# Performance work log

Hardware: AMD Instinct MI355X
Metric: run time of the kernel (lower is better)

Reference implementation:

```python
import jax, jax.numpy as jnp
import numpy as np

MEM_SIZE = 1_000_000
DIM = 128
BS = 256
K = 1024
TEMP = 0.07
MOM_V = 0.5
MOM_A = 0.5


def _l2norm(x, axis=-1, eps=1e-12):
    n = jnp.sqrt(jnp.sum(x * x, axis=axis, keepdims=True))
    return x / jnp.maximum(n, eps)


def setup_inputs() -> dict:
    key = jax.random.key(0)
    k1, k2, k3, k4, k5, k6 = jax.random.split(key, 6)
    video_emb = jax.random.normal(k1, (BS, DIM), dtype=jnp.float32)
    audio_emb = jax.random.normal(k2, (BS, DIM), dtype=jnp.float32)
    y = jax.random.randint(k3, (BS,), 0, MEM_SIZE, dtype=jnp.int32)
    # alias method draws over memory_size-1 items (before shifting past y)
    neg_idx = jax.random.randint(k4, (BS, K), 0, MEM_SIZE - 1, dtype=jnp.int32)
    view1_mem = _l2norm(jax.random.normal(k5, (MEM_SIZE, DIM), dtype=jnp.float32))
    view2_mem = _l2norm(jax.random.normal(k6, (MEM_SIZE, DIM), dtype=jnp.float32))
    return {
        "video_emb": video_emb,
        "audio_emb": audio_emb,
        "y": y,
        "neg_idx": neg_idx,
        "view1_mem": view1_mem,
        "view2_mem": view2_mem,
    }


def reference(video_emb, audio_emb, y, neg_idx, view1_mem, view2_mem):
    v = _l2norm(video_emb, axis=1)   # [bs, dim]
    a = _l2norm(audio_emb, axis=1)   # [bs, dim]

    # shift negative indices past the positive index y (as in sample_negatives)
    idx = neg_idx + (neg_idx >= y[:, None]).astype(neg_idx.dtype)  # [bs, K]

    # gather positives / negatives from memory banks
    v_pos = view1_mem[y]           # [bs, dim]
    a_pos = view2_mem[y]           # [bs, dim]
    v_neg = view1_mem[idx]         # [bs, K, dim]
    a_neg = view2_mem[idx]         # [bs, K, dim]

    # xModal scores (wModal=False)
    v2a_pos = jnp.einsum("bd,bd->b", a_pos, v)[:, None] / TEMP    # [bs, 1]
    v2a_neg = jnp.einsum("bkd,bd->bk", a_neg, v) / TEMP           # [bs, K]
    a2v_pos = jnp.einsum("bd,bd->b", v_pos, a)[:, None] / TEMP    # [bs, 1]
    a2v_neg = jnp.einsum("bkd,bd->bk", v_neg, a) / TEMP           # [bs, K]

    scores = jnp.stack(
        [jnp.concatenate([v2a_pos, v2a_neg], axis=1),
         jnp.concatenate([a2v_pos, a2v_neg], axis=1)],
        axis=0,
    )  # [2, bs, K+1]

    # momentum scatter update of memory banks (no_grad in original)
    new1 = _l2norm(MOM_V * v_pos + (1.0 - MOM_V) * v, axis=1)
    new2 = _l2norm(MOM_A * a_pos + (1.0 - MOM_A) * a, axis=1)
    view1_new = view1_mem.at[y].set(new1)
    view2_new = view2_mem.at[y].set(new2)

    return scores, view1_new, view2_new
```

## Files before the change

kernel.cpp:

```cpp
#include <hip/hip_runtime.h>

#define MEM_SIZE 1000000
#define DIM 128
#define BS 256
#define K 1024
#define NSC (K + 1)

constexpr float INV_TEMP = 1.0f / 0.07f;
constexpr float MOM = 0.5f;

#define TOTAL_BLOCKS 2048
#define COPY_BLOCKS  1536

typedef float fx4 __attribute__((ext_vector_type(4)));

__device__ __forceinline__ float wave_reduce_sum(float v) {
    #pragma unroll
    for (int off = 32; off > 0; off >>= 1)
        v += __shfl_xor(v, off, 64);
    return v;
}

__global__ __launch_bounds__(256) void fused_kernel(
    const float* __restrict__ video, const float* __restrict__ audio,
    const int* __restrict__ y, const int* __restrict__ neg,
    const float* __restrict__ view1, const float* __restrict__ view2,
    float* __restrict__ scores,
    fx4* __restrict__ out1, fx4* __restrict__ out2) {
    const int bid = blockIdx.x;
    const int tid = threadIdx.x;

    if ((bid & 3) == 0) {
        const int bm = bid >> 2;
        const int m = bm >> 8;
        const int b = bm & (BS - 1);
        const int lane = tid & 63;
        const int wv = tid >> 6;
        const int yb = y[b];

        const float* emb = (m == 0) ? video : audio;
        const float2 e = reinterpret_cast<const float2*>(emb + b * DIM)[lane];
        const float ss = wave_reduce_sum(e.x * e.x + e.y * e.y);
        const float inv = 1.0f / fmaxf(sqrtf(ss), 1e-12f);
        const float vx = e.x * inv, vy = e.y * inv;

        const float2* mem2 =
            reinterpret_cast<const float2*>((m == 0) ? view2 : view1);
        float* srow = scores + (size_t)bm * NSC;
        const int* nb = neg + b * K;

        const int chunk = (NSC + 3) / 4;
        const int j0 = wv * chunk;
        const int j1 = min(NSC, j0 + chunk);

        int j = j0;
        for (; j + 1 < j1; j += 2) {
            int r0;
            if (j == 0) r0 = yb;
            else { const int ni = nb[j - 1]; r0 = ni + (ni >= yb ? 1 : 0); }
            const int ni1 = nb[j];
            const int r1 = ni1 + (ni1 >= yb ? 1 : 0);
            const float2 x0 = mem2[(size_t)r0 * 64 + lane];
            const float2 x1 = mem2[(size_t)r1 * 64 + lane];
            const float s0 = wave_reduce_sum(x0.x * vx + x0.y * vy);
            const float s1 = wave_reduce_sum(x1.x * vx + x1.y * vy);
            if (lane == 0) {
                srow[j] = s0 * INV_TEMP;
                srow[j + 1] = s1 * INV_TEMP;
            }
        }
        if (j < j1) {
            int r0;
            if (j == 0) r0 = yb;
            else { const int ni = nb[j - 1]; r0 = ni + (ni >= yb ? 1 : 0); }
            const float2 x0 = mem2[(size_t)r0 * 64 + lane];
            const float s0 = wave_reduce_sum(x0.x * vx + x0.y * vy);
            if (lane == 0) srow[j] = s0 * INV_TEMP;
        }
    } else {
        const long long n4 = (long long)MEM_SIZE * DIM / 4;
        const int cb = bid - (bid >> 2) - 1;
        const fx4* s1 = reinterpret_cast<const fx4*>(view1);
        const fx4* s2 = reinterpret_cast<const fx4*>(view2);
        long long i = (long long)cb * blockDim.x + tid;
        const long long stride = (long long)COPY_BLOCKS * blockDim.x;
        for (; i < n4; i += stride) {
            const fx4 a = __builtin_nontemporal_load(&s1[i]);
            const fx4 c = __builtin_nontemporal_load(&s2[i]);
            __builtin_nontemporal_store(a, &out1[i]);
            __builtin_nontemporal_store(c, &out2[i]);
        }
    }
}

__global__ void scatter_kernel(const float* __restrict__ video,
                               const float* __restrict__ audio,
                               const int* __restrict__ y,
                               const float* __restrict__ view1,
                               const float* __restrict__ view2,
                               float* __restrict__ out1,
                               float* __restrict__ out2) {
    const int blk = blockIdx.x;
    const int lane = threadIdx.x;
    const int bank = blk >> 8;
    const int b = blk & (BS - 1);
    const int row = y[b];
    for (int b2 = b + 1; b2 < BS; ++b2)
        if (y[b2] == row) return;

    const float* emb = (bank == 0) ? video : audio;
    const float2 e = reinterpret_cast<const float2*>(emb + b * DIM)[lane];
    const float ss = wave_reduce_sum(e.x * e.x + e.y * e.y);
    const float inv = 1.0f / fmaxf(sqrtf(ss), 1e-12f);
    const float vx = e.x * inv, vy = e.y * inv;

    const float* mem = (bank == 0) ? view1 : view2;
    const float2 xp =
        reinterpret_cast<const float2*>(mem + (size_t)row * DIM)[lane];
    float2 nv = make_float2(MOM * xp.x + (1.0f - MOM) * vx,
                            MOM * xp.y + (1.0f - MOM) * vy);
    const float ss2 = wave_reduce_sum(nv.x * nv.x + nv.y * nv.y);
    const float inv2 = 1.0f / fmaxf(sqrtf(ss2), 1e-12f);
    float* out = (bank == 0) ? out1 : out2;
    reinterpret_cast<float2*>(out + (size_t)row * DIM)[lane] =
        make_float2(nv.x * inv2, nv.y * inv2);
}

extern "C" void kernel_launch(void* const* d_in, const int* in_sizes, int n_in,
                              void* d_out, int out_size, void* d_ws, size_t ws_size,
                              hipStream_t stream) {
    const float* video = (const float*)d_in[0];
    const float* audio = (const float*)d_in[1];
    const int* y       = (const int*)d_in[2];
    const int* neg     = (const int*)d_in[3];
    const float* v1    = (const float*)d_in[4];
    const float* v2    = (const float*)d_in[5];

    float* out    = (float*)d_out;
    float* scores = out;
    float* out1   = out + 2 * BS * NSC;
    float* out2   = out1 + (size_t)MEM_SIZE * DIM;

    fused_kernel<<<TOTAL_BLOCKS, 256, 0, stream>>>(
        video, audio, y, neg, v1, v2,
        scores, (fx4*)out1, (fx4*)out2);

    scatter_kernel<<<2 * BS, 64, 0, stream>>>(video, audio, y, v1, v2,
                                              out1, out2);
}
```

Before: 428.1 us.

## Interleave gather scoring into copy loop to hit cache on recently streamed rows

Every block now both copies the memory banks and computes its slice of negative scores. Each lane packs its gathered row index and score slot into a key and scores a row only after the copy front has passed it by a margin. The idea is to serve the gather reads from cache lines the copy just brought in, instead of making separate random DRAM reads, and to balance work across all blocks. Copy loads become regular (cached) loads instead of nontemporal ones. This adds ballot/shuffle overhead inside the copy loop and uneven per-iteration work, and it depends on blocks progressing in rough lockstep for the cache hits to happen.

```diff
diff --git a/kernel.cpp b/kernel.cpp
--- a/kernel.cpp
+++ b/kernel.cpp
@@ -9,8 +9,10 @@
 constexpr float INV_TEMP = 1.0f / 0.07f;
 constexpr float MOM = 0.5f;
 
-#define TOTAL_BLOCKS 2048
-#define COPY_BLOCKS  1536
+#define NB 2048
+#define BT 128
+#define STRIDE ((long long)NB * BT)
+#define MARGIN_ROWS 24576
 
 typedef float fx4 __attribute__((ext_vector_type(4)));
 
@@ -21,7 +23,26 @@
     return v;
 }
 
-__global__ __launch_bounds__(256) void fused_kernel(
+__device__ __forceinline__ void drain(unsigned key, bool& done, int rmax,
+                                      const float2* __restrict__ gmem,
+                                      float qx, float qy,
+                                      float* __restrict__ srow, int lane) {
+    const bool rdy = !done && (int)(key >> 11) < rmax;
+    unsigned long long msk = __ballot(rdy);
+    while (msk) {
+        const int src = __ffsll((long long)msk) - 1;
+        msk &= msk - 1;
+        const unsigned k = (unsigned)__shfl((int)key, src, 64);
+        const int row = (int)(k >> 11);
+        const int j = (int)(k & 2047u);
+        const float2 x = gmem[(size_t)row * 64 + lane];
+        const float sc = wave_reduce_sum(x.x * qx + x.y * qy);
+        if (lane == src) srow[j] = sc * INV_TEMP;
+    }
+    done = done || rdy;
+}
+
+__global__ __launch_bounds__(BT, 4) void fused_kernel(
     const float* __restrict__ video, const float* __restrict__ audio,
     const int* __restrict__ y, const int* __restrict__ neg,
     const float* __restrict__ view1, const float* __restrict__ view2,
@@ -29,67 +50,57 @@
     fx4* __restrict__ out1, fx4* __restrict__ out2) {
     const int bid = blockIdx.x;
     const int tid = threadIdx.x;
+    const int lane = tid & 63;
+    const int wv = tid >> 6;
+    const int u = bid >> 2;
+    const int s = bid & 3;
+    const int m = u >> 8;
+    const int b = u & (BS - 1);
+    const int yb = y[b];
 
-    if ((bid & 3) == 0) {
-        const int bm = bid >> 2;
-        const int m = bm >> 8;
-        const int b = bm & (BS - 1);
-        const int lane = tid & 63;
-        const int wv = tid >> 6;
-        const int yb = y[b];
+    const float* emb = (m == 0) ? video : audio;
+    const float2 e = reinterpret_cast<const float2*>(emb + b * DIM)[lane];
+    const float ss = wave_reduce_sum(e.x * e.x + e.y * e.y);
+    const float qinv = 1.0f / fmaxf(sqrtf(ss), 1e-12f);
+    const float qx = e.x * qinv, qy = e.y * qinv;
 
-        const float* emb = (m == 0) ? video : audio;
-        const float2 e = reinterpret_cast<const float2*>(emb + b * DIM)[lane];
-        const float ss = wave_reduce_sum(e.x * e.x + e.y * e.y);
-        const float inv = 1.0f / fmaxf(sqrtf(ss), 1e-12f);
-        const float vx = e.x * inv, vy = e.y * inv;
+    const int jbase = 1 + s * 256 + wv * 128;
+    const int j0 = jbase + lane;
+    const int j1 = jbase + 64 + lane;
+    const int ni0 = neg[b * K + j0 - 1];
+    const int ni1 = neg[b * K + j1 - 1];
+    const int r0 = ni0 + (ni0 >= yb ? 1 : 0);
+    const int r1 = ni1 + (ni1 >= yb ? 1 : 0);
+    const unsigned key0 = ((unsigned)r0 << 11) | (unsigned)j0;
+    const unsigned key1 = ((unsigned)r1 << 11) | (unsigned)j1;
+    bool done0 = false, done1 = false;
 
-        const float2* mem2 =
-            reinterpret_cast<const float2*>((m == 0) ? view2 : view1);
-        float* srow = scores + (size_t)bm * NSC;
-        const int* nb = neg + b * K;
+    const float2* gmem =
+        reinterpret_cast<const float2*>((m == 0) ? view2 : view1);
+    float* srow = scores + (size_t)u * NSC;
 
-        const int chunk = (NSC + 3) / 4;
-        const int j0 = wv * chunk;
-        const int j1 = min(NSC, j0 + chunk);
+    const fx4* s1 = reinterpret_cast<const fx4*>(view1);
+    const fx4* s2 = reinterpret_cast<const fx4*>(view2);
 
-        int j = j0;
-        for (; j + 1 < j1; j += 2) {
-            int r0;
-            if (j == 0) r0 = yb;
-            else { const int ni = nb[j - 1]; r0 = ni + (ni >= yb ? 1 : 0); }
-            const int ni1 = nb[j];
-            const int r1 = ni1 + (ni1 >= yb ? 1 : 0);
-            const float2 x0 = mem2[(size_t)r0 * 64 + lane];
-            const float2 x1 = mem2[(size_t)r1 * 64 + lane];
-            const float s0 = wave_reduce_sum(x0.x * vx + x0.y * vy);
-            const float s1 = wave_reduce_sum(x1.x * vx + x1.y * vy);
-            if (lane == 0) {
-                srow[j] = s0 * INV_TEMP;
-                srow[j + 1] = s1 * INV_TEMP;
-            }
-        }
-        if (j < j1) {
-            int r0;
-            if (j == 0) r0 = yb;
-            else { const int ni = nb[j - 1]; r0 = ni + (ni >= yb ? 1 : 0); }
-            const float2 x0 = mem2[(size_t)r0 * 64 + lane];
-            const float s0 = wave_reduce_sum(x0.x * vx + x0.y * vy);
-            if (lane == 0) srow[j] = s0 * INV_TEMP;
-        }
-    } else {
-        const long long n4 = (long long)MEM_SIZE * DIM / 4;
-        const int cb = bid - (bid >> 2) - 1;
-        const fx4* s1 = reinterpret_cast<const fx4*>(view1);
-        const fx4* s2 = reinterpret_cast<const fx4*>(view2);
-        long long i = (long long)cb * blockDim.x + tid;
-        const long long stride = (long long)COPY_BLOCKS * blockDim.x;
-        for (; i < n4; i += stride) {
-            const fx4 a = __builtin_nontemporal_load(&s1[i]);
-            const fx4 c = __builtin_nontemporal_load(&s2[i]);
-            __builtin_nontemporal_store(a, &out1[i]);
-            __builtin_nontemporal_store(c, &out2[i]);
-        }
+    const long long n4 = (long long)MEM_SIZE * DIM / 4;
+    long long i = (long long)bid * BT + tid;
+    long long ibase = (long long)bid * BT;
+    for (; i < n4; i += STRIDE, ibase += STRIDE) {
+        const fx4 a = s1[i];
+        const fx4 c = s2[i];
+        __builtin_nontemporal_store(a, &out1[i]);
+        __builtin_nontemporal_store(c, &out2[i]);
+        const int rmax = (int)(ibase >> 5) - MARGIN_ROWS;
+        drain(key0, done0, rmax, gmem, qx, qy, srow, lane);
+        drain(key1, done1, rmax, gmem, qx, qy, srow, lane);
+    }
+    drain(key0, done0, 0x7fffffff, gmem, qx, qy, srow, lane);
+    drain(key1, done1, 0x7fffffff, gmem, qx, qy, srow, lane);
+
+    if (s == 0 && wv == 0) {
+        const float2 x = gmem[(size_t)yb * 64 + lane];
+        const float sc = wave_reduce_sum(x.x * qx + x.y * qy);
+        if (lane == 0) srow[0] = sc * INV_TEMP;
     }
 }
 
@@ -141,7 +152,7 @@
     float* out1   = out + 2 * BS * NSC;
     float* out2   = out1 + (size_t)MEM_SIZE * DIM;
 
-    fused_kernel<<<TOTAL_BLOCKS, 256, 0, stream>>>(
+    fused_kernel<<<NB, BT, 0, stream>>>(
         video, audio, y, neg, v1, v2,
         scores, (fx4*)out1, (fx4*)out2);
 
```

Measured after the change: 406.5 us. 1.05x faster.

## Invert gather into per-row inverted index and compute scores during bank copy

Applied to the files above, without the earlier changes.

Builds an inverted index (row -> list of (batch, slot) keys) via atomics in workspace, then computes all positive and negative scores while streaming the memory banks for the copy. Each bank row is read once and reused for every score that needs it, replacing the random gathers. Rows with more than four references overflow into a list handled by a tail kernel. This adds three extra kernel launches, a 4 MB counts zeroing pass and atomic contention, and keeps the old path as a fallback when the workspace is too small.

```diff
diff --git a/kernel.cpp b/kernel.cpp
--- a/kernel.cpp
+++ b/kernel.cpp
@@ -5,14 +5,24 @@
 #define BS 256
 #define K 1024
 #define NSC (K + 1)
+#define CAP 4
+#define OVFCAP 32768
 
 constexpr float INV_TEMP = 1.0f / 0.07f;
 constexpr float MOM = 0.5f;
 
-#define TOTAL_BLOCKS 2048
-#define COPY_BLOCKS  1536
+#define NB 2048
+#define BT 256
+#define NWAVES (NB * BT / 64)
 
 typedef float fx4 __attribute__((ext_vector_type(4)));
+
+#define QTAB_OFF 0
+#define CNT_OFF  262144
+#define SLOT_OFF 4262144
+#define OVFC_OFF 20262144
+#define OVF_OFF  20262400
+#define WS_NEED  20524544
 
 __device__ __forceinline__ float wave_reduce_sum(float v) {
     #pragma unroll
@@ -21,7 +31,166 @@
     return v;
 }
 
-__global__ __launch_bounds__(256) void fused_kernel(
+__global__ void normzero_kernel(const float* __restrict__ video,
+                                const float* __restrict__ audio,
+                                float* __restrict__ qtab,
+                                int* __restrict__ counts,
+                                int* __restrict__ ovf_cnt) {
+    const int u = blockIdx.x;
+    const int lane = threadIdx.x;
+    const int b = u & (BS - 1);
+    const float* src = (u < BS) ? video : audio;
+    const float2 e = reinterpret_cast<const float2*>(src + b * DIM)[lane];
+    const float ss = wave_reduce_sum(e.x * e.x + e.y * e.y);
+    const float inv = 1.0f / fmaxf(sqrtf(ss), 1e-12f);
+    reinterpret_cast<float2*>(qtab + u * DIM)[lane] =
+        make_float2(e.x * inv, e.y * inv);
+    for (int i = u * 64 + lane; i < MEM_SIZE; i += 512 * 64) counts[i] = 0;
+    if (u == 0 && lane == 0) *ovf_cnt = 0;
+}
+
+__global__ void build_kernel(const int* __restrict__ y,
+                             const int* __restrict__ neg,
+                             int* __restrict__ counts,
+                             int* __restrict__ slots,
+                             int* __restrict__ ovf_cnt,
+                             int2* __restrict__ ovf) {
+    const int E = blockIdx.x * blockDim.x + threadIdx.x;
+    int b, j, row;
+    if (E < BS * K) {
+        b = E >> 10;
+        const int jj = E & 1023;
+        j = jj + 1;
+        const int ni = neg[b * K + jj];
+        const int yb = y[b];
+        row = ni + (ni >= yb ? 1 : 0);
+    } else {
+        b = E - BS * K;
+        if (b >= BS) return;
+        j = 0;
+        row = y[b];
+    }
+    const int key = (b << 11) | j;
+    const int old = atomicAdd(&counts[row], 1);
+    if (old < CAP) {
+        slots[row * CAP + old] = key;
+    } else {
+        const int p = atomicAdd(ovf_cnt, 1);
+        if (p < OVFCAP) ovf[p] = make_int2(row, key);
+    }
+}
+
+__global__ __launch_bounds__(BT) void main_kernel(
+    const float* __restrict__ view1, const float* __restrict__ view2,
+    const float* __restrict__ qtab, const int* __restrict__ counts,
+    const int* __restrict__ slots,
+    float* __restrict__ scores,
+    fx4* __restrict__ out1, fx4* __restrict__ out2) {
+    const int tid = blockIdx.x * BT + threadIdx.x;
+    const int wid = tid >> 6;
+    const int lane = tid & 63;
+    const int half = lane >> 5;
+    const int hl = lane & 31;
+    const fx4* s1 = reinterpret_cast<const fx4*>(view1);
+    const fx4* s2 = reinterpret_cast<const fx4*>(view2);
+    const fx4* qt4 = reinterpret_cast<const fx4*>(qtab);
+
+    const long long n4 = (long long)MEM_SIZE * DIM / 4;
+    for (long long wbase = (long long)wid * 64; wbase < n4;
+         wbase += (long long)NWAVES * 64) {
+        const long long i = wbase + lane;
+        const fx4 a = s1[i];
+        const fx4 c = s2[i];
+        __builtin_nontemporal_store(a, &out1[i]);
+        __builtin_nontemporal_store(c, &out2[i]);
+
+        const int row = (int)(wbase >> 5) + half;
+        int cnt = counts[row];
+        if (cnt > CAP) cnt = CAP;
+        for (int t = 0; t < cnt; ++t) {
+            const int key = slots[row * CAP + t];
+            const int b = key >> 11;
+            const int j = key & 2047;
+            const fx4 q0 = qt4[b * 32 + hl];
+            const fx4 q1 = qt4[(256 + b) * 32 + hl];
+            float d0 = q0.x * c.x + q0.y * c.y + q0.z * c.z + q0.w * c.w;
+            float d1 = q1.x * a.x + q1.y * a.y + q1.z * a.z + q1.w * a.w;
+            #pragma unroll
+            for (int off = 16; off > 0; off >>= 1) {
+                d0 += __shfl_xor(d0, off, 64);
+                d1 += __shfl_xor(d1, off, 64);
+            }
+            if (hl == 0) {
+                scores[b * NSC + j] = d0 * INV_TEMP;
+                scores[(256 + b) * NSC + j] = d1 * INV_TEMP;
+            }
+        }
+    }
+}
+
+__global__ void tail_kernel(const float* __restrict__ video,
+                            const float* __restrict__ audio,
+                            const int* __restrict__ y,
+                            const float* __restrict__ view1,
+                            const float* __restrict__ view2,
+                            const float* __restrict__ qtab,
+                            const int* __restrict__ ovf_cnt,
+                            const int2* __restrict__ ovf,
+                            float* __restrict__ scores,
+                            float* __restrict__ out1,
+                            float* __restrict__ out2) {
+    const int blk = blockIdx.x;
+    const int lane = threadIdx.x;
+    if (blk < 512) {
+        const int bank = blk >> 8;
+        const int b = blk & (BS - 1);
+        const int row = y[b];
+        for (int b2 = b + 1; b2 < BS; ++b2)
+            if (y[b2] == row) return;
+        const float* emb = (bank == 0) ? video : audio;
+        const float2 e = reinterpret_cast<const float2*>(emb + b * DIM)[lane];
+        const float ss = wave_reduce_sum(e.x * e.x + e.y * e.y);
+        const float inv = 1.0f / fmaxf(sqrtf(ss), 1e-12f);
+        const float* mem = (bank == 0) ? view1 : view2;
+        const float2 xp =
+            reinterpret_cast<const float2*>(mem + (size_t)row * DIM)[lane];
+        float2 nv = make_float2(MOM * xp.x + (1.0f - MOM) * e.x * inv,
+                                MOM * xp.y + (1.0f - MOM) * e.y * inv);
+        const float ss2 = wave_reduce_sum(nv.x * nv.x + nv.y * nv.y);
+        const float inv2 = 1.0f / fmaxf(sqrtf(ss2), 1e-12f);
+        float* out = (bank == 0) ? out1 : out2;
+        reinterpret_cast<float2*>(out + (size_t)row * DIM)[lane] =
+            make_float2(nv.x * inv2, nv.y * inv2);
+    } else {
+        int n = *ovf_cnt;
+        if (n > OVFCAP) n = OVFCAP;
+        const float2* m1 = reinterpret_cast<const float2*>(view1);
+        const float2* m2 = reinterpret_cast<const float2*>(view2);
+        const float2* qt2 = reinterpret_cast<const float2*>(qtab);
+        for (int e = blk - 512; e < n; e += 128) {
+            const int2 rk = ovf[e];
+            const int row = rk.x, key = rk.y;
+            const int b = key >> 11, j = key & 2047;
+            const float2 xa = m1[(size_t)row * 64 + lane];
+            const float2 xc = m2[(size_t)row * 64 + lane];
+            const float2 q0 = qt2[(size_t)b * 64 + lane];
+            const float2 q1 = qt2[(size_t)(256 + b) * 64 + lane];
+            float d0 = xc.x * q0.x + xc.y * q0.y;
+            float d1 = xa.x * q1.x + xa.y * q1.y;
+            #pragma unroll
+            for (int off = 32; off > 0; off >>= 1) {
+                d0 += __shfl_xor(d0, off, 64);
+                d1 += __shfl_xor(d1, off, 64);
+            }
+            if (lane == 0) {
+                scores[b * NSC + j] = d0 * INV_TEMP;
+                scores[(256 + b) * NSC + j] = d1 * INV_TEMP;
+            }
+        }
+    }
+}
+
+__global__ __launch_bounds__(256) void fb_fused(
     const float* __restrict__ video, const float* __restrict__ audio,
     const int* __restrict__ y, const int* __restrict__ neg,
     const float* __restrict__ view1, const float* __restrict__ view2,
@@ -29,7 +198,6 @@
     fx4* __restrict__ out1, fx4* __restrict__ out2) {
     const int bid = blockIdx.x;
     const int tid = threadIdx.x;
-
     if ((bid & 3) == 0) {
         const int bm = bid >> 2;
         const int m = bm >> 8;
@@ -37,39 +205,19 @@
         const int lane = tid & 63;
         const int wv = tid >> 6;
         const int yb = y[b];
-
         const float* emb = (m == 0) ? video : audio;
         const float2 e = reinterpret_cast<const float2*>(emb + b * DIM)[lane];
         const float ss = wave_reduce_sum(e.x * e.x + e.y * e.y);
         const float inv = 1.0f / fmaxf(sqrtf(ss), 1e-12f);
         const float vx = e.x * inv, vy = e.y * inv;
-
         const float2* mem2 =
             reinterpret_cast<const float2*>((m == 0) ? view2 : view1);
         float* srow = scores + (size_t)bm * NSC;
         const int* nb = neg + b * K;
-
         const int chunk = (NSC + 3) / 4;
         const int j0 = wv * chunk;
         const int j1 = min(NSC, j0 + chunk);
-
-        int j = j0;
-        for (; j + 1 < j1; j += 2) {
-            int r0;
-            if (j == 0) r0 = yb;
-            else { const int ni = nb[j - 1]; r0 = ni + (ni >= yb ? 1 : 0); }
-            const int ni1 = nb[j];
-            const int r1 = ni1 + (ni1 >= yb ? 1 : 0);
-            const float2 x0 = mem2[(size_t)r0 * 64 + lane];
-            const float2 x1 = mem2[(size_t)r1 * 64 + lane];
-            const float s0 = wave_reduce_sum(x0.x * vx + x0.y * vy);
-            const float s1 = wave_reduce_sum(x1.x * vx + x1.y * vy);
-            if (lane == 0) {
-                srow[j] = s0 * INV_TEMP;
-                srow[j + 1] = s1 * INV_TEMP;
-            }
-        }
-        if (j < j1) {
+        for (int j = j0; j < j1; ++j) {
             int r0;
             if (j == 0) r0 = yb;
             else { const int ni = nb[j - 1]; r0 = ni + (ni >= yb ? 1 : 0); }
@@ -83,7 +231,7 @@
         const fx4* s1 = reinterpret_cast<const fx4*>(view1);
         const fx4* s2 = reinterpret_cast<const fx4*>(view2);
         long long i = (long long)cb * blockDim.x + tid;
-        const long long stride = (long long)COPY_BLOCKS * blockDim.x;
+        const long long stride = (long long)1536 * blockDim.x;
         for (; i < n4; i += stride) {
             const fx4 a = __builtin_nontemporal_load(&s1[i]);
             const fx4 c = __builtin_nontemporal_load(&s2[i]);
@@ -93,13 +241,13 @@
     }
 }
 
-__global__ void scatter_kernel(const float* __restrict__ video,
-                               const float* __restrict__ audio,
-                               const int* __restrict__ y,
-                               const float* __restrict__ view1,
-                               const float* __restrict__ view2,
-                               float* __restrict__ out1,
-                               float* __restrict__ out2) {
+__global__ void fb_scatter(const float* __restrict__ video,
+                           const float* __restrict__ audio,
+                           const int* __restrict__ y,
+                           const float* __restrict__ view1,
+                           const float* __restrict__ view2,
+                           float* __restrict__ out1,
+                           float* __restrict__ out2) {
     const int blk = blockIdx.x;
     const int lane = threadIdx.x;
     const int bank = blk >> 8;
@@ -107,18 +255,15 @@
     const int row = y[b];
     for (int b2 = b + 1; b2 < BS; ++b2)
         if (y[b2] == row) return;
-
     const float* emb = (bank == 0) ? video : audio;
     const float2 e = reinterpret_cast<const float2*>(emb + b * DIM)[lane];
     const float ss = wave_reduce_sum(e.x * e.x + e.y * e.y);
     const float inv = 1.0f / fmaxf(sqrtf(ss), 1e-12f);
-    const float vx = e.x * inv, vy = e.y * inv;
-
     const float* mem = (bank == 0) ? view1 : view2;
     const float2 xp =
         reinterpret_cast<const float2*>(mem + (size_t)row * DIM)[lane];
-    float2 nv = make_float2(MOM * xp.x + (1.0f - MOM) * vx,
-                            MOM * xp.y + (1.0f - MOM) * vy);
+    float2 nv = make_float2(MOM * xp.x + (1.0f - MOM) * e.x * inv,
+                            MOM * xp.y + (1.0f - MOM) * e.y * inv);
     const float ss2 = wave_reduce_sum(nv.x * nv.x + nv.y * nv.y);
     const float inv2 = 1.0f / fmaxf(sqrtf(ss2), 1e-12f);
     float* out = (bank == 0) ? out1 : out2;
@@ -141,10 +286,24 @@
     float* out1   = out + 2 * BS * NSC;
     float* out2   = out1 + (size_t)MEM_SIZE * DIM;
 
-    fused_kernel<<<TOTAL_BLOCKS, 256, 0, stream>>>(
-        video, audio, y, neg, v1, v2,
-        scores, (fx4*)out1, (fx4*)out2);
-
-    scatter_kernel<<<2 * BS, 64, 0, stream>>>(video, audio, y, v1, v2,
-                                              out1, out2);
-}
+    if (ws_size < (size_t)WS_NEED) {
+        fb_fused<<<2048, 256, 0, stream>>>(video, audio, y, neg, v1, v2,
+                                           scores, (fx4*)out1, (fx4*)out2);
+        fb_scatter<<<512, 64, 0, stream>>>(video, audio, y, v1, v2, out1, out2);
+        return;
+    }
+
+    char* ws = (char*)d_ws;
+    float* qtab  = (float*)(ws + QTAB_OFF);
+    int* counts  = (int*)(ws + CNT_OFF);
+    int* slots   = (int*)(ws + SLOT_OFF);
+    int* ovf_cnt = (int*)(ws + OVFC_OFF);
+    int2* ovf    = (int2*)(ws + OVF_OFF);
+
+    normzero_kernel<<<512, 64, 0, stream>>>(video, audio, qtab, counts, ovf_cnt);
+    build_kernel<<<1025, 256, 0, stream>>>(y, neg, counts, slots, ovf_cnt, ovf);
+    main_kernel<<<NB, BT, 0, stream>>>(v1, v2, qtab, counts, slots,
+                                       scores, (fx4*)out1, (fx4*)out2);
+    tail_kernel<<<640, 64, 0, stream>>>(video, audio, y, v1, v2, qtab,
+                                        ovf_cnt, ovf, scores, out1, out2);
+}
```

After: 470.6 us. 9.9% more time.
